# Kernel tuning notes

Measured on AMD Instinct MI355X. Metric: run time of the kernel, lower is better.

Reference implementation:

```python
import jax, jax.numpy as jnp
import numpy as np


def log_g(x):
    # torch: where(x>=0, log(relu(x)+0.5), -softplus(-x))
    return jnp.where(x >= 0, jnp.log(jnp.maximum(x, 0.0) + 0.5), -jax.nn.softplus(-x))


def parallel_scan_log(log_coeffs, log_values):
    # Faithful to source: cumsum over LAST (feature) dim, then pad time dim
    # (axis=1) with one leading zero row; logcumsumexp over time dim (axis=1).
    a_star = jnp.cumsum(log_coeffs, axis=-1)                      # [B,T,D]
    a_star = jnp.pad(a_star, ((0, 0), (1, 0), (0, 0)))            # [B,T+1,D]
    log_h0_plus_b_star = jax.lax.cumlogsumexp(log_values - a_star, axis=1)
    return jnp.exp(a_star + log_h0_plus_b_star)                   # [B,T+1,D]


def setup_inputs() -> dict:
    key = jax.random.key(0)
    ks = jax.random.split(key, 8)
    B, T, Din, Dout = 8, 4096, 1024, 1024
    scale = 1.0 / np.sqrt(Din)
    return {
        "x": jax.random.normal(ks[0], (B, T, Din), dtype=jnp.float32),
        "h_0": jax.random.uniform(ks[1], (B, 1, Dout), dtype=jnp.float32),
        "Wi": jax.random.uniform(ks[2], (Dout, Din), jnp.float32, -scale, scale),
        "bi": jax.random.uniform(ks[3], (Dout,), jnp.float32, -scale, scale),
        "Wf": jax.random.uniform(ks[4], (Dout, Din), jnp.float32, -scale, scale),
        "bf": jax.random.uniform(ks[5], (Dout,), jnp.float32, -scale, scale),
        "Wh": jax.random.uniform(ks[6], (Dout, Din), jnp.float32, -scale, scale),
        "bh": jax.random.uniform(ks[7], (Dout,), jnp.float32, -scale, scale),
    }


def reference(x, h_0, Wi, bi, Wf, bf, Wh, bh):
    # gate pre-activations: [B,T,Dout]
    zi = jnp.einsum('btd,od->bto', x, Wi) + bi
    zf = jnp.einsum('btd,od->bto', x, Wf) + bf
    zh = jnp.einsum('btd,od->bto', x, Wh) + bh
    diff = jax.nn.softplus(-zf) - jax.nn.softplus(-zi)
    log_f = -jax.nn.softplus(diff)
    log_i = -jax.nn.softplus(-diff)
    log_values = jnp.concatenate([log_g(h_0), log_i + log_g(zh)], axis=1)  # [B,T+1,D]
    return parallel_scan_log(log_f, log_values)
```

## Files before the change

kernel.cpp:

```cpp
#include <hip/hip_runtime.h>
#include <math.h>
#include <stdint.h>

#define B_    8
#define T_    4096
#define TP1   4097
#define D_    1024
#define K_    1024
#define M_    32768

#define BLK_M 128
#define BLK_N 64
#define BK    32

#define TC    64
#define NC    65

typedef __attribute__((ext_vector_type(8))) _Float16 f16x8;
typedef __attribute__((ext_vector_type(4))) float    f32x4;

__device__ __forceinline__ float sp_f(float x) {
    return fmaxf(x, 0.0f) + __logf(1.0f + __expf(-fabsf(x)));
}
__device__ __forceinline__ float log_g_f(float x) {
    return (x >= 0.0f) ? __logf(x + 0.5f) : x - __logf(1.0f + __expf(x));
}

__device__ __forceinline__ void g2lds16(const void* g, void* l) {
    __builtin_amdgcn_global_load_lds(
        (const __attribute__((address_space(1))) uint32_t*)g,
        (__attribute__((address_space(3))) uint32_t*)l,
        16, 0, 0);
}

__global__ __launch_bounds__(256) void k_cvt_x(
    const float* __restrict__ X, _Float16* __restrict__ Xs)
{
    int g = blockIdx.x * 256 + threadIdx.x;
    int l = g & 63;
    int frag = g >> 6;
    int kt = frag & 31;
    int mt = frag >> 5;
    int m = (mt << 4) + (l & 15);
    int k = (kt << 5) + ((l >> 4) << 3);
    const float4* p = (const float4*)&X[(size_t)m * K_ + k];
    float4 a = p[0], b = p[1];
    f16x8 h;
    h[0]=(_Float16)a.x; h[1]=(_Float16)a.y; h[2]=(_Float16)a.z; h[3]=(_Float16)a.w;
    h[4]=(_Float16)b.x; h[5]=(_Float16)b.y; h[6]=(_Float16)b.z; h[7]=(_Float16)b.w;
    *(f16x8*)&Xs[(size_t)g * 8] = h;
}

__global__ __launch_bounds__(256) void k_cvt_w(
    const float* __restrict__ Wi, const float* __restrict__ Wf,
    const float* __restrict__ Wh, _Float16* __restrict__ Ws)
{
    int g = blockIdx.x * 256 + threadIdx.x;
    int mat = g >> 17;
    int r = g & 131071;
    const float* W = (mat == 0) ? Wi : (mat == 1) ? Wf : Wh;
    int l = r & 63;
    int frag = r >> 6;
    int kt = frag & 31;
    int nt = frag >> 5;
    int n = (nt << 4) + (l & 15);
    int k = (kt << 5) + ((l >> 4) << 3);
    const float4* p = (const float4*)&W[(size_t)n * K_ + k];
    float4 a = p[0], b = p[1];
    f16x8 h;
    h[0]=(_Float16)a.x; h[1]=(_Float16)a.y; h[2]=(_Float16)a.z; h[3]=(_Float16)a.w;
    h[4]=(_Float16)b.x; h[5]=(_Float16)b.y; h[6]=(_Float16)b.z; h[7]=(_Float16)b.w;
    *(f16x8*)&Ws[(size_t)g * 8] = h;
}

__device__ __forceinline__ void stage_tile(
    const _Float16* Ag, const _Float16* Bg, int kt,
    _Float16* lAbuf, _Float16* lBbuf, int fa0, int fb0)
{
    g2lds16(Ag + (size_t)(fa0 * 32 + kt) * 512,       lAbuf + fa0 * 512);
    g2lds16(Ag + (size_t)((fa0 + 1) * 32 + kt) * 512, lAbuf + (fa0 + 1) * 512);
#pragma unroll
    for (int j = 0; j < 3; ++j) {
        int fb  = fb0 + j;
        int mat = fb >> 2, nf = fb & 3;
        g2lds16(Bg + ((size_t)mat * 2048 + (size_t)nf * 32 + kt) * 512,
                lBbuf + fb * 512);
    }
}

__device__ __forceinline__ void compute_tile(
    const _Float16* lAbuf, const _Float16* lBbuf,
    int wm, int wnf, int lane, f32x4 acc[3][4][2])
{
    f16x8 af[4];
#pragma unroll
    for (int mt = 0; mt < 4; ++mt)
        af[mt] = *(const f16x8*)&lAbuf[((wm >> 4) + mt) * 512 + lane * 8];
    __builtin_amdgcn_s_setprio(1);
#pragma unroll
    for (int a = 0; a < 3; ++a) {
#pragma unroll
        for (int nt = 0; nt < 2; ++nt) {
            f16x8 bfr = *(const f16x8*)&lBbuf[(a * 4 + wnf + nt) * 512 + lane * 8];
#pragma unroll
            for (int mt = 0; mt < 4; ++mt)
                acc[a][mt][nt] = __builtin_amdgcn_mfma_f32_16x16x32_f16(
                    af[mt], bfr, acc[a][mt][nt], 0, 0, 0);
        }
    }
    __builtin_amdgcn_s_setprio(0);
}

#define WAITBAR(N) do {                                         \
    asm volatile("s_waitcnt vmcnt(" #N ")" ::: "memory");       \
    __builtin_amdgcn_s_barrier();                               \
} while (0)

__global__ __launch_bounds__(256) void k_gemm(
    const _Float16* __restrict__ Xs, const _Float16* __restrict__ Ws,
    const float* __restrict__ bi, const float* __restrict__ bfv,
    const float* __restrict__ bh,
    float* __restrict__ ws_a, float* __restrict__ out)
{
    __shared__ __align__(16) _Float16 lA[3][8 * 512];
    __shared__ __align__(16) _Float16 lB[3][12 * 512];

    const int tid  = threadIdx.x;
    const int lane = tid & 63;
    const int w    = tid >> 6;

    const int bid = blockIdx.y * (int)gridDim.x + blockIdx.x;
    const int cpx = ((int)gridDim.x * (int)gridDim.y) >> 3;
    const int swz = (bid & 7) * cpx + (bid >> 3);
    const int n0  = (swz & 15) * BLK_N;
    const int m0  = (swz >> 4) * BLK_M;

    const int wm   = (w >> 1) * 64;
    const int wnf  = (w & 1) * 2;
    const int l16  = lane & 15;
    const int q    = lane >> 4;

    const int fa0 = w * 2;
    const int fb0 = w * 3;

    const _Float16* Ag = Xs + ((size_t)(m0 >> 4) * 32) * 512 + (size_t)lane * 8;
    const _Float16* Bg = Ws + (size_t)(n0 >> 4) * 32 * 512 + (size_t)lane * 8;

    f32x4 acc[3][4][2];
#pragma unroll
    for (int a = 0; a < 3; ++a)
#pragma unroll
        for (int mt = 0; mt < 4; ++mt)
#pragma unroll
            for (int nt = 0; nt < 2; ++nt) acc[a][mt][nt] = (f32x4)(0.0f);

    stage_tile(Ag, Bg, 0, lA[0], lB[0], fa0, fb0);
    stage_tile(Ag, Bg, 1, lA[1], lB[1], fa0, fb0);
    WAITBAR(5);

    for (int it = 0; it < 10; ++it) {
        const int kt = it * 3;

        stage_tile(Ag, Bg, kt + 2, lA[2], lB[2], fa0, fb0);
        compute_tile(lA[0], lB[0], wm, wnf, lane, acc);
        WAITBAR(5);

        stage_tile(Ag, Bg, kt + 3, lA[0], lB[0], fa0, fb0);
        compute_tile(lA[1], lB[1], wm, wnf, lane, acc);
        WAITBAR(5);

        stage_tile(Ag, Bg, kt + 4, lA[1], lB[1], fa0, fb0);
        compute_tile(lA[2], lB[2], wm, wnf, lane, acc);
        WAITBAR(5);
    }
    compute_tile(lA[0], lB[0], wm, wnf, lane, acc);
    WAITBAR(0);
    compute_tile(lA[1], lB[1], wm, wnf, lane, acc);

#pragma unroll
    for (int mt = 0; mt < 4; ++mt) {
#pragma unroll
        for (int nt = 0; nt < 2; ++nt) {
            int n = n0 + (wnf + nt) * 16 + l16;
            float biv = bi[n], bfvv = bfv[n], bhv = bh[n];
#pragma unroll
            for (int r = 0; r < 4; ++r) {
                int m = m0 + wm + mt * 16 + q * 4 + r;
                float zi = acc[0][mt][nt][r] + biv;
                float zf = acc[1][mt][nt][r] + bfvv;
                float zh = acc[2][mt][nt][r] + bhv;
                float spf = fmaxf(-zf, 0.0f) + __logf(1.0f + __expf(-fabsf(zf)));
                float spi = fmaxf(-zi, 0.0f) + __logf(1.0f + __expf(-fabsf(zi)));
                float df  = spf - spi;
                float spd = fmaxf(df, 0.0f) + __logf(1.0f + __expf(-fabsf(df)));
                float lf  = -spd;
                float li  = df - spd;
                float lg  = (zh >= 0.0f) ? __logf(zh + 0.5f)
                                         : zh - __logf(1.0f + __expf(zh));
                float lv  = li + lg;
                ws_a[(size_t)m * D_ + n] = lf;
                int b = m >> 12;
                out[(size_t)(m + b + 1) * D_ + n] = lv;
            }
        }
    }
}

__global__ __launch_bounds__(256) void k_cumsum(
    float* __restrict__ ws_a, float* __restrict__ out)
{
    const int tid  = threadIdx.x;
    const int lane = tid & 63;
    const int row  = blockIdx.x * 4 + (tid >> 6);
    const int b    = row >> 12;
    float* pa = ws_a + (size_t)row * D_;
    float* pu = out + (size_t)(row + b + 1) * D_;

    float vals[16];
#pragma unroll
    for (int j = 0; j < 4; ++j) {
        float4 v = *(const float4*)&pa[lane * 16 + j * 4];
        vals[j*4+0] = v.x; vals[j*4+1] = v.y; vals[j*4+2] = v.z; vals[j*4+3] = v.w;
    }
    float s = 0.0f;
#pragma unroll
    for (int j = 0; j < 16; ++j) s += vals[j];
    float inc = s;
#pragma unroll
    for (int off = 1; off < 64; off <<= 1) {
        float nv = __shfl_up(inc, off);
        if (lane >= off) inc += nv;
    }
    float run = inc - s;
#pragma unroll
    for (int j = 0; j < 16; ++j) { run += vals[j]; vals[j] = run; }
#pragma unroll
    for (int j = 0; j < 4; ++j) {
        float4 lv4 = *(const float4*)&pu[lane * 16 + j * 4];
        float4 a4; a4.x = vals[j*4]; a4.y = vals[j*4+1]; a4.z = vals[j*4+2]; a4.w = vals[j*4+3];
        float4 u4; u4.x = lv4.x - a4.x; u4.y = lv4.y - a4.y;
                   u4.z = lv4.z - a4.z; u4.w = lv4.w - a4.w;
        *(float4*)&pa[lane * 16 + j * 4] = a4;
        *(float4*)&pu[lane * 16 + j * 4] = u4;
    }
}

__global__ void k_h0(const float* __restrict__ h0, float* __restrict__ out)
{
    int i = blockIdx.x * 256 + threadIdx.x;
    int b = i >> 10, d = i & 1023;
    out[(size_t)b * TP1 * D_ + d] = log_g_f(h0[i]);
}

__global__ __launch_bounds__(256) void k_chunk(
    const float* __restrict__ out, float* __restrict__ ctm, float* __restrict__ cts)
{
    int c = blockIdx.x, b = blockIdx.y;
    int d = threadIdx.x * 4;
    int t0 = c * TC, t1 = min(TP1, t0 + TC);
    float4 m = make_float4(-__builtin_inff(), -__builtin_inff(),
                           -__builtin_inff(), -__builtin_inff());
    float4 s = make_float4(0.f, 0.f, 0.f, 0.f);
    const float* p = out + ((size_t)b * TP1 + t0) * D_ + d;
    for (int t = t0; t < t1; ++t) {
        float4 u = *(const float4*)p; p += D_;
        float4 mn;
        mn.x = fmaxf(m.x, u.x); mn.y = fmaxf(m.y, u.y);
        mn.z = fmaxf(m.z, u.z); mn.w = fmaxf(m.w, u.w);
        s.x = s.x * __expf(m.x - mn.x) + __expf(u.x - mn.x);
        s.y = s.y * __expf(m.y - mn.y) + __expf(u.y - mn.y);
        s.z = s.z * __expf(m.z - mn.z) + __expf(u.z - mn.z);
        s.w = s.w * __expf(m.w - mn.w) + __expf(u.w - mn.w);
        m = mn;
    }
    int ci = (b * NC + c) * D_ + d;
    *(float4*)&ctm[ci] = m; *(float4*)&cts[ci] = s;
}

__global__ __launch_bounds__(256) void k_carry(
    const float* __restrict__ ctm, const float* __restrict__ cts,
    float* __restrict__ carry)
{
    int i = blockIdx.x * 256 + threadIdx.x;
    int b = i >> 10, d = i & 1023;
    float m = -__builtin_inff(), s = 0.0f;
    for (int c = 0; c < NC; ++c) {
        int ci = (b * NC + c) * D_ + d;
        carry[ci] = (s == 0.0f) ? -__builtin_inff() : (m + __logf(s));
        float m2 = ctm[ci], s2 = cts[ci];
        float M = fmaxf(m, m2);
        s = s * __expf(m - M) + s2 * __expf(m2 - M);
        m = M;
    }
}

__global__ __launch_bounds__(256) void k_final(
    const float* __restrict__ ws_a, const float* __restrict__ carry,
    float* __restrict__ out)
{
    int c = blockIdx.x, b = blockIdx.y;
    int d = threadIdx.x * 4;
    int t0 = c * TC, t1 = min(TP1, t0 + TC);
    float4 v = *(const float4*)&carry[(b * NC + c) * D_ + d];
    float4 m, s;
    m.x = v.x; s.x = (v.x == -__builtin_inff()) ? 0.f : 1.f;
    m.y = v.y; s.y = (v.y == -__builtin_inff()) ? 0.f : 1.f;
    m.z = v.z; s.z = (v.z == -__builtin_inff()) ? 0.f : 1.f;
    m.w = v.w; s.w = (v.w == -__builtin_inff()) ? 0.f : 1.f;
    for (int t = t0; t < t1; ++t) {
        size_t oi = ((size_t)b * TP1 + t) * D_ + d;
        float4 u = *(const float4*)&out[oi];
        float4 mn;
        mn.x = fmaxf(m.x, u.x); mn.y = fmaxf(m.y, u.y);
        mn.z = fmaxf(m.z, u.z); mn.w = fmaxf(m.w, u.w);
        s.x = s.x * __expf(m.x - mn.x) + __expf(u.x - mn.x);
        s.y = s.y * __expf(m.y - mn.y) + __expf(u.y - mn.y);
        s.z = s.z * __expf(m.z - mn.z) + __expf(u.z - mn.z);
        s.w = s.w * __expf(m.w - mn.w) + __expf(u.w - mn.w);
        m = mn;
        float4 a = make_float4(0.f, 0.f, 0.f, 0.f);
        if (t != 0) a = *(const float4*)&ws_a[((size_t)b * T_ + (t - 1)) * D_ + d];
        float4 o;
        o.x = __expf(a.x + mn.x) * s.x;
        o.y = __expf(a.y + mn.y) * s.y;
        o.z = __expf(a.z + mn.z) * s.z;
        o.w = __expf(a.w + mn.w) * s.w;
        *(float4*)&out[oi] = o;
    }
}

extern "C" void kernel_launch(void* const* d_in, const int* in_sizes, int n_in,
                              void* d_out, int out_size, void* d_ws, size_t ws_size,
                              hipStream_t stream)
{
    const float* X   = (const float*)d_in[0];
    const float* h0  = (const float*)d_in[1];
    const float* Wi  = (const float*)d_in[2];
    const float* bi  = (const float*)d_in[3];
    const float* Wf  = (const float*)d_in[4];
    const float* bfv = (const float*)d_in[5];
    const float* Wh  = (const float*)d_in[6];
    const float* bh  = (const float*)d_in[7];
    float* out  = (float*)d_out;

    char* wsb = (char*)d_ws;
    float*    ws_a = (float*)wsb;
    _Float16* Xs   = (_Float16*)(wsb + (size_t)M_ * D_ * 4);
    _Float16* Wsv  = (_Float16*)(wsb + (size_t)M_ * D_ * 4 + (size_t)M_ * K_ * 2);
    float* ctm   = (float*)(wsb + (size_t)M_ * D_ * 4);
    float* cts   = ctm + B_ * NC * D_;
    float* carry = cts + B_ * NC * D_;

    k_cvt_x<<<M_ * K_ / 8 / 256, 256, 0, stream>>>(X, Xs);
    k_cvt_w<<<3 * D_ * K_ / 8 / 256, 256, 0, stream>>>(Wi, Wf, Wh, Wsv);

    dim3 g1(D_ / BLK_N, M_ / BLK_M);
    k_gemm<<<g1, 256, 0, stream>>>(Xs, Wsv, bi, bfv, bh, ws_a, out);
    k_h0<<<32, 256, 0, stream>>>(h0, out);
    k_cumsum<<<M_ / 4, 256, 0, stream>>>(ws_a, out);
    k_chunk<<<dim3(NC, B_), 256, 0, stream>>>(out, ctm, cts);
    k_carry<<<32, 256, 0, stream>>>(ctm, cts, carry);
    k_final<<<dim3(NC, B_), 256, 0, stream>>>(ws_a, carry, out);
}
```

Measured before the change: 804.6 us.

## Fuse cumsum with chunk logsumexp, deepen GEMM pipeline, simplify gate math

Merges the feature-dim cumsum kernel with the per-chunk logsumexp reduction, so the log-values are reduced while still in registers instead of being re-read from global memory. Chunk boundaries are realigned so chunk 0 holds only the h0 row, which k_h0 now seeds directly. The GEMM moves to a 4-stage LDS pipeline with a new grouped tile swizzle. The softplus gate math is replaced by an algebraically equivalent form that needs fewer exp/log calls. Together these add LDS use and register pressure, and the new gate formula can overflow when exp(-z) gets large.

```diff
diff --git a/kernel.cpp b/kernel.cpp
--- a/kernel.cpp
+++ b/kernel.cpp
@@ -13,15 +13,12 @@
 #define BLK_N 64
 #define BK    32
 
-#define TC    64
+#define CH    64
 #define NC    65
 
 typedef __attribute__((ext_vector_type(8))) _Float16 f16x8;
 typedef __attribute__((ext_vector_type(4))) float    f32x4;
 
-__device__ __forceinline__ float sp_f(float x) {
-    return fmaxf(x, 0.0f) + __logf(1.0f + __expf(-fabsf(x)));
-}
 __device__ __forceinline__ float log_g_f(float x) {
     return (x >= 0.0f) ? __logf(x + 0.5f) : x - __logf(1.0f + __expf(x));
 }
@@ -122,18 +119,24 @@
     const float* __restrict__ bh,
     float* __restrict__ ws_a, float* __restrict__ out)
 {
-    __shared__ __align__(16) _Float16 lA[3][8 * 512];
-    __shared__ __align__(16) _Float16 lB[3][12 * 512];
+    __shared__ __align__(16) _Float16 lA[4][8 * 512];
+    __shared__ __align__(16) _Float16 lB[4][12 * 512];
 
     const int tid  = threadIdx.x;
     const int lane = tid & 63;
     const int w    = tid >> 6;
 
     const int bid = blockIdx.y * (int)gridDim.x + blockIdx.x;
-    const int cpx = ((int)gridDim.x * (int)gridDim.y) >> 3;
-    const int swz = (bid & 7) * cpx + (bid >> 3);
-    const int n0  = (swz & 15) * BLK_N;
-    const int m0  = (swz >> 4) * BLK_M;
+    const int x   = bid & 7;
+    const int j   = bid >> 3;
+    const int jj  = j & 63;
+    const int g   = j >> 6;
+    const int gn  = g & 1;
+    const int gm  = g >> 1;
+    const int tile_n = gn * 8 + (jj & 7);
+    const int tile_m = x * 32 + gm * 8 + (jj >> 3);
+    const int n0  = tile_n * BLK_N;
+    const int m0  = tile_m * BLK_M;
 
     const int wm   = (w >> 1) * 64;
     const int wnf  = (w & 1) * 2;
@@ -156,26 +159,35 @@
 
     stage_tile(Ag, Bg, 0, lA[0], lB[0], fa0, fb0);
     stage_tile(Ag, Bg, 1, lA[1], lB[1], fa0, fb0);
+    stage_tile(Ag, Bg, 2, lA[2], lB[2], fa0, fb0);
+    WAITBAR(10);
+
+    for (int it = 0; it < 7; ++it) {
+        const int kt = it * 4;
+        stage_tile(Ag, Bg, kt + 3, lA[3], lB[3], fa0, fb0);
+        compute_tile(lA[0], lB[0], wm, wnf, lane, acc);
+        WAITBAR(10);
+
+        stage_tile(Ag, Bg, kt + 4, lA[0], lB[0], fa0, fb0);
+        compute_tile(lA[1], lB[1], wm, wnf, lane, acc);
+        WAITBAR(10);
+
+        stage_tile(Ag, Bg, kt + 5, lA[1], lB[1], fa0, fb0);
+        compute_tile(lA[2], lB[2], wm, wnf, lane, acc);
+        WAITBAR(10);
+
+        stage_tile(Ag, Bg, kt + 6, lA[2], lB[2], fa0, fb0);
+        compute_tile(lA[3], lB[3], wm, wnf, lane, acc);
+        WAITBAR(10);
+    }
+    stage_tile(Ag, Bg, 31, lA[3], lB[3], fa0, fb0);
+    compute_tile(lA[0], lB[0], wm, wnf, lane, acc);
+    WAITBAR(10);
+    compute_tile(lA[1], lB[1], wm, wnf, lane, acc);
     WAITBAR(5);
-
-    for (int it = 0; it < 10; ++it) {
-        const int kt = it * 3;
-
-        stage_tile(Ag, Bg, kt + 2, lA[2], lB[2], fa0, fb0);
-        compute_tile(lA[0], lB[0], wm, wnf, lane, acc);
-        WAITBAR(5);
-
-        stage_tile(Ag, Bg, kt + 3, lA[0], lB[0], fa0, fb0);
-        compute_tile(lA[1], lB[1], wm, wnf, lane, acc);
-        WAITBAR(5);
-
-        stage_tile(Ag, Bg, kt + 4, lA[1], lB[1], fa0, fb0);
-        compute_tile(lA[2], lB[2], wm, wnf, lane, acc);
-        WAITBAR(5);
-    }
-    compute_tile(lA[0], lB[0], wm, wnf, lane, acc);
+    compute_tile(lA[2], lB[2], wm, wnf, lane, acc);
     WAITBAR(0);
-    compute_tile(lA[1], lB[1], wm, wnf, lane, acc);
+    compute_tile(lA[3], lB[3], wm, wnf, lane, acc);
 
 #pragma unroll
     for (int mt = 0; mt < 4; ++mt) {
@@ -189,15 +201,14 @@
                 float zi = acc[0][mt][nt][r] + biv;
                 float zf = acc[1][mt][nt][r] + bfvv;
                 float zh = acc[2][mt][nt][r] + bhv;
-                float spf = fmaxf(-zf, 0.0f) + __logf(1.0f + __expf(-fabsf(zf)));
-                float spi = fmaxf(-zi, 0.0f) + __logf(1.0f + __expf(-fabsf(zi)));
-                float df  = spf - spi;
-                float spd = fmaxf(df, 0.0f) + __logf(1.0f + __expf(-fabsf(df)));
-                float lf  = -spd;
-                float li  = df - spd;
-                float lg  = (zh >= 0.0f) ? __logf(zh + 0.5f)
-                                         : zh - __logf(1.0f + __expf(zh));
-                float lv  = li + lg;
+                float ei = __expf(-zi), ef = __expf(-zf);
+                float Pi = 1.0f + ei,  Pf = 1.0f + ef;
+                float lS = __logf(Pi + Pf);
+                float lf = __logf(Pi) - lS;
+                float li = __logf(Pf) - lS;
+                float lg = (zh >= 0.0f) ? __logf(zh + 0.5f)
+                                        : zh - __logf(1.0f + __expf(zh));
+                float lv = li + lg;
                 ws_a[(size_t)m * D_ + n] = lf;
                 int b = m >> 12;
                 out[(size_t)(m + b + 1) * D_ + n] = lv;
@@ -206,75 +217,104 @@
     }
 }
 
-__global__ __launch_bounds__(256) void k_cumsum(
-    float* __restrict__ ws_a, float* __restrict__ out)
-{
+__global__ __launch_bounds__(256) void k_cumchunk(
+    float* __restrict__ ws_a, float* __restrict__ out,
+    float* __restrict__ ctm, float* __restrict__ cts)
+{
+    const int c    = blockIdx.x;
+    const int b    = blockIdx.y;
     const int tid  = threadIdx.x;
     const int lane = tid & 63;
-    const int row  = blockIdx.x * 4 + (tid >> 6);
-    const int b    = row >> 12;
-    float* pa = ws_a + (size_t)row * D_;
-    float* pu = out + (size_t)(row + b + 1) * D_;
-
-    float vals[16];
-#pragma unroll
-    for (int j = 0; j < 4; ++j) {
-        float4 v = *(const float4*)&pa[lane * 16 + j * 4];
-        vals[j*4+0] = v.x; vals[j*4+1] = v.y; vals[j*4+2] = v.z; vals[j*4+3] = v.w;
-    }
-    float s = 0.0f;
-#pragma unroll
-    for (int j = 0; j < 16; ++j) s += vals[j];
-    float inc = s;
-#pragma unroll
-    for (int off = 1; off < 64; off <<= 1) {
-        float nv = __shfl_up(inc, off);
-        if (lane >= off) inc += nv;
-    }
-    float run = inc - s;
-#pragma unroll
-    for (int j = 0; j < 16; ++j) { run += vals[j]; vals[j] = run; }
-#pragma unroll
-    for (int j = 0; j < 4; ++j) {
-        float4 lv4 = *(const float4*)&pu[lane * 16 + j * 4];
-        float4 a4; a4.x = vals[j*4]; a4.y = vals[j*4+1]; a4.z = vals[j*4+2]; a4.w = vals[j*4+3];
-        float4 u4; u4.x = lv4.x - a4.x; u4.y = lv4.y - a4.y;
-                   u4.z = lv4.z - a4.z; u4.w = lv4.w - a4.w;
-        *(float4*)&pa[lane * 16 + j * 4] = a4;
-        *(float4*)&pu[lane * 16 + j * 4] = u4;
-    }
-}
-
-__global__ void k_h0(const float* __restrict__ h0, float* __restrict__ out)
+    const int w    = tid >> 6;
+
+    __shared__ float smm[4][1024];
+    __shared__ float sss[4][1024];
+
+    float cm[16], cs[16];
+#pragma unroll
+    for (int j = 0; j < 16; ++j) { cm[j] = -__builtin_inff(); cs[j] = 0.0f; }
+
+    const int r0 = c * CH + w * 16;
+    for (int i = 0; i < 16; ++i) {
+        const int r = r0 + i;
+        float* pa = ws_a + ((size_t)b * T_ + r) * D_;
+        float* pu = out + ((size_t)b * TP1 + r + 1) * D_;
+
+        float vals[16];
+#pragma unroll
+        for (int j = 0; j < 4; ++j) {
+            float4 v = *(const float4*)&pa[lane * 16 + j * 4];
+            vals[j*4+0]=v.x; vals[j*4+1]=v.y; vals[j*4+2]=v.z; vals[j*4+3]=v.w;
+        }
+        float s = 0.0f;
+#pragma unroll
+        for (int j = 0; j < 16; ++j) s += vals[j];
+        float inc = s;
+#pragma unroll
+        for (int off = 1; off < 64; off <<= 1) {
+            float nv = __shfl_up(inc, off);
+            if (lane >= off) inc += nv;
+        }
+        float run = inc - s;
+#pragma unroll
+        for (int j = 0; j < 16; ++j) { run += vals[j]; vals[j] = run; }
+
+#pragma unroll
+        for (int j = 0; j < 4; ++j) {
+            float4 lv4 = *(const float4*)&pu[lane * 16 + j * 4];
+            float4 a4; a4.x = vals[j*4]; a4.y = vals[j*4+1];
+                       a4.z = vals[j*4+2]; a4.w = vals[j*4+3];
+            float4 u4; u4.x = lv4.x - a4.x; u4.y = lv4.y - a4.y;
+                       u4.z = lv4.z - a4.z; u4.w = lv4.w - a4.w;
+            *(float4*)&pa[lane * 16 + j * 4] = a4;
+            *(float4*)&pu[lane * 16 + j * 4] = u4;
+            float uu[4] = {u4.x, u4.y, u4.z, u4.w};
+#pragma unroll
+            for (int e = 0; e < 4; ++e) {
+                int jj = j * 4 + e;
+                float mn = fmaxf(cm[jj], uu[e]);
+                cs[jj] = cs[jj] * __expf(cm[jj] - mn) + __expf(uu[e] - mn);
+                cm[jj] = mn;
+            }
+        }
+    }
+
+#pragma unroll
+    for (int j = 0; j < 16; ++j) {
+        smm[w][lane * 16 + j] = cm[j];
+        sss[w][lane * 16 + j] = cs[j];
+    }
+    __syncthreads();
+
+    {
+        int d0 = tid * 4;
+        size_t ci = ((size_t)b * NC + 1 + c) * D_ + d0;
+#pragma unroll
+        for (int e = 0; e < 4; ++e) {
+            int d = d0 + e;
+            float M = smm[0][d], S = sss[0][d];
+#pragma unroll
+            for (int ww = 1; ww < 4; ++ww) {
+                float m2 = smm[ww][d], s2 = sss[ww][d];
+                float Mn = fmaxf(M, m2);
+                S = S * __expf(M - Mn) + s2 * __expf(m2 - Mn);
+                M = Mn;
+            }
+            ctm[ci + e] = M;
+            cts[ci + e] = S;
+        }
+    }
+}
+
+__global__ void k_h0(const float* __restrict__ h0, float* __restrict__ out,
+                     float* __restrict__ ctm, float* __restrict__ cts)
 {
     int i = blockIdx.x * 256 + threadIdx.x;
     int b = i >> 10, d = i & 1023;
-    out[(size_t)b * TP1 * D_ + d] = log_g_f(h0[i]);
-}
-
-__global__ __launch_bounds__(256) void k_chunk(
-    const float* __restrict__ out, float* __restrict__ ctm, float* __restrict__ cts)
-{
-    int c = blockIdx.x, b = blockIdx.y;
-    int d = threadIdx.x * 4;
-    int t0 = c * TC, t1 = min(TP1, t0 + TC);
-    float4 m = make_float4(-__builtin_inff(), -__builtin_inff(),
-                           -__builtin_inff(), -__builtin_inff());
-    float4 s = make_float4(0.f, 0.f, 0.f, 0.f);
-    const float* p = out + ((size_t)b * TP1 + t0) * D_ + d;
-    for (int t = t0; t < t1; ++t) {
-        float4 u = *(const float4*)p; p += D_;
-        float4 mn;
-        mn.x = fmaxf(m.x, u.x); mn.y = fmaxf(m.y, u.y);
-        mn.z = fmaxf(m.z, u.z); mn.w = fmaxf(m.w, u.w);
-        s.x = s.x * __expf(m.x - mn.x) + __expf(u.x - mn.x);
-        s.y = s.y * __expf(m.y - mn.y) + __expf(u.y - mn.y);
-        s.z = s.z * __expf(m.z - mn.z) + __expf(u.z - mn.z);
-        s.w = s.w * __expf(m.w - mn.w) + __expf(u.w - mn.w);
-        m = mn;
-    }
-    int ci = (b * NC + c) * D_ + d;
-    *(float4*)&ctm[ci] = m; *(float4*)&cts[ci] = s;
+    float u0 = log_g_f(h0[i]);
+    out[(size_t)b * TP1 * D_ + d] = u0;
+    ctm[(size_t)b * NC * D_ + d] = u0;
+    cts[(size_t)b * NC * D_ + d] = 1.0f;
 }
 
 __global__ __launch_bounds__(256) void k_carry(
@@ -285,7 +325,7 @@
     int b = i >> 10, d = i & 1023;
     float m = -__builtin_inff(), s = 0.0f;
     for (int c = 0; c < NC; ++c) {
-        int ci = (b * NC + c) * D_ + d;
+        size_t ci = ((size_t)b * NC + c) * D_ + d;
         carry[ci] = (s == 0.0f) ? -__builtin_inff() : (m + __logf(s));
         float m2 = ctm[ci], s2 = cts[ci];
         float M = fmaxf(m, m2);
@@ -300,8 +340,9 @@
 {
     int c = blockIdx.x, b = blockIdx.y;
     int d = threadIdx.x * 4;
-    int t0 = c * TC, t1 = min(TP1, t0 + TC);
-    float4 v = *(const float4*)&carry[(b * NC + c) * D_ + d];
+    int t0 = (c == 0) ? 0 : ((c - 1) * CH + 1);
+    int t1 = (c == 0) ? 1 : (c * CH + 1);
+    float4 v = *(const float4*)&carry[((size_t)b * NC + c) * D_ + d];
     float4 m, s;
     m.x = v.x; s.x = (v.x == -__builtin_inff()) ? 0.f : 1.f;
     m.y = v.y; s.y = (v.y == -__builtin_inff()) ? 0.f : 1.f;
@@ -356,9 +397,8 @@
 
     dim3 g1(D_ / BLK_N, M_ / BLK_M);
     k_gemm<<<g1, 256, 0, stream>>>(Xs, Wsv, bi, bfv, bh, ws_a, out);
-    k_h0<<<32, 256, 0, stream>>>(h0, out);
-    k_cumsum<<<M_ / 4, 256, 0, stream>>>(ws_a, out);
-    k_chunk<<<dim3(NC, B_), 256, 0, stream>>>(out, ctm, cts);
+    k_h0<<<32, 256, 0, stream>>>(h0, out, ctm, cts);
+    k_cumchunk<<<dim3(T_ / CH, B_), 256, 0, stream>>>(ws_a, out, ctm, cts);
     k_carry<<<32, 256, 0, stream>>>(ctm, cts, carry);
     k_final<<<dim3(NC, B_), 256, 0, stream>>>(ws_a, carry, out);
 }
```

New measurement: 1.021 ms. 1.27x slower.
